# Kernel optimization log

Hardware: AMD Instinct MI355X
Metric: run time of the kernel (lower is better)

Reference implementation:

```python
import math
import jax, jax.numpy as jnp
from jax import lax
import numpy as np

EPS = 1e-07
GAMMA = 2.2
FOV = 10.0
SPEC_ALPHA_MAX = 128.0
SHADOW_CAP = 0.1
SHADOW_SMOOTH = 7


def _grid_sample_border(img, grid):
    # img: [B,1,H,W]; grid: [B,H,W,2], grid[...,0]=x (width), grid[...,1]=y (height),
    # normalized to [-1,1], align_corners=False, padding_mode='border' (torch semantics).
    B, _, H, W = img.shape
    x = (grid[..., 0] + 1.0) * (W / 2.0) - 0.5
    y = (grid[..., 1] + 1.0) * (H / 2.0) - 0.5
    x0 = jnp.floor(x)
    y0 = jnp.floor(y)
    wx = x - x0
    wy = y - y0
    x0i = jnp.clip(x0.astype(jnp.int32), 0, W - 1)
    x1i = jnp.clip(x0.astype(jnp.int32) + 1, 0, W - 1)
    y0i = jnp.clip(y0.astype(jnp.int32), 0, H - 1)
    y1i = jnp.clip(y0.astype(jnp.int32) + 1, 0, H - 1)
    im = img[:, 0]  # [B,H,W]
    bidx = jnp.arange(B)[:, None, None]
    v00 = im[bidx, y0i, x0i]
    v01 = im[bidx, y0i, x1i]
    v10 = im[bidx, y1i, x0i]
    v11 = im[bidx, y1i, x1i]
    out = (v00 * (1 - wx) * (1 - wy) + v01 * wx * (1 - wy)
           + v10 * (1 - wx) * wy + v11 * wx * wy)
    return out[:, None]  # [B,1,H,W]


def compute_shadow(depth, light_dir, fov=FOV):
    # Iterative shadow ray-march: image_size grid_sample steps along -light_dir.
    depth = lax.stop_gradient(depth)          # original detaches
    light_dir = lax.stop_gradient(light_dir)
    B, _, S, _ = depth.shape
    t = math.tan(fov / 360.0 * math.pi)
    c = jnp.linspace(-1.0, 1.0, S, dtype=depth.dtype) * t
    xx, yy = jnp.meshgrid(c, c, indexing='ij')  # torch.meshgrid default ij
    dirs = jnp.stack([yy, xx, jnp.ones_like(xx)], axis=0)[None]  # [1,3,S,S]
    pos0 = dirs * depth                                          # [B,3,S,S]
    step = -light_dir.reshape(B, 3, 1, 1) / S

    def body(i, carry):
        pos, sh = carry
        pos = pos + step
        pix = pos[:, :2] / pos[:, 2:3] / t           # [B,2,S,S]
        grid = jnp.transpose(pix, (0, 2, 3, 1))      # [B,S,S,2]
        sampled = _grid_sample_border(depth, grid)
        sh = sh | (sampled - pos[:, 2:3] < 0)
        return (pos, sh)

    _, sh = lax.fori_loop(0, S, body, (pos0, jnp.zeros(depth.shape, dtype=bool)))
    return sh


def _gaussian_blur(x, ksize=SHADOW_SMOOTH, sigma=2.0):
    r = (ksize - 1) / 2.0
    g = np.exp(-((np.arange(ksize) - r) ** 2) / (2.0 * sigma ** 2))
    k2 = np.outer(g, g)
    k2 = (k2 / k2.sum()).astype(np.float32)
    kern = jnp.asarray(k2)[None, None]  # [1,1,k,k]
    return lax.conv_general_dilated(x, kern, (1, 1), 'SAME',
                                    dimension_numbers=('NCHW', 'OIHW', 'NCHW'))


def _get_view_d(fov, S):
    t = math.tan(fov / 360.0 * math.pi)
    x = jnp.linspace(-1.0, 1.0, S, dtype=jnp.float32) * t
    xx, yy = jnp.meshgrid(x, x, indexing='ij')
    v = jnp.stack([yy, xx, jnp.ones_like(xx)], axis=0)  # [3,S,S]
    v = v / jnp.linalg.norm(v, axis=0, keepdims=True)
    v = v[:, ::-1, ::-1]  # flip([1,2])
    return v[None]  # [1,3,S,S]


def _border_mask(S, margin=5):
    m = jnp.zeros((S, S), dtype=jnp.float32)
    m = m.at[margin:S - margin, margin:S - margin].set(1.0)
    return m[None, None]


def setup_inputs() -> dict:
    key = jax.random.key(0)
    k1, k2, k3, k4, k5 = jax.random.split(key, 5)
    B, S = 32, 256
    netA_out = jax.random.normal(k1, (B, 5, S, S), dtype=jnp.float32)
    netL_out = jax.random.normal(k2, (B, 6), dtype=jnp.float32)
    n = jax.random.normal(k3, (B, 3, S, S), dtype=jnp.float32)
    recon_normal = n / jnp.linalg.norm(n, axis=1, keepdims=True)
    recon_depth = jax.random.uniform(k4, (B, 1, S, S), dtype=jnp.float32) * 0.5 + 0.75
    light = jax.random.normal(k5, (B, 2), dtype=jnp.float32)
    return {"netA_out": netA_out, "netL_out": netL_out,
            "recon_normal": recon_normal, "recon_depth": recon_depth,
            "light": light}


def reference(netA_out, netL_out, recon_normal, recon_depth, light):
    b, _, S, _ = netA_out.shape
    t_alpha = math.sqrt(SPEC_ALPHA_MAX) - 1.0

    recon_albedo_specular = jnp.tanh(netA_out)
    recon_albedo = (recon_albedo_specular[:, :3] / 2 + 0.5) ** GAMMA  # to_gamma_space

    recon_light = jnp.tanh(netL_out)  # [B,6]
    # spec_alpha: tanh of netL_out[:, :1], rescaled to [1, spec_alpha_max]
    sa = jnp.tanh(netL_out[:, :1]).reshape(b, 1, 1, 1)
    spec_alpha = ((sa * 0.5 + 0.5) * t_alpha + 1.0) ** 2
    spec_strength = (recon_light[:, 5:6].reshape(b, 1, 1, 1) * 0.5 + 0.5) * 0.5

    light_a = (recon_light[:, 1:2] / 2 + 0.5).reshape(b, 1, 1, 1)
    light_b = (recon_light[:, 2:3] / 2 + 0.5).reshape(b, 1, 1, 1)
    # light has shape [B,2] -> concat z=1, then normalize
    light_d = jnp.concatenate([light, jnp.ones((b, 1), dtype=light.dtype)], axis=1)
    light_d = light_d / jnp.linalg.norm(light_d, axis=1, keepdims=True)

    view_d = _get_view_d(FOV, S)
    ld = light_d[:, :, None, None]
    cos_theta = jnp.sum(recon_normal * ld, axis=1, keepdims=True)
    diffuse = jnp.clip(cos_theta, 0.0)

    mask = _border_mask(S, 5)
    reflect_d = 2.0 * cos_theta * recon_normal - ld
    specular = (jnp.clip(jnp.sum(view_d * reflect_d, axis=1, keepdims=True), 0.0)
                * (cos_theta > 0).astype(jnp.float32) * mask)
    spec_shading = jnp.clip(specular, EPS, 1.0 - EPS) ** spec_alpha

    is_shadow = compute_shadow(recon_depth, light_d).astype(jnp.float32)
    shadow_s = _gaussian_blur(is_shadow)
    shadow_factor = jnp.clip(1.0 - shadow_s, SHADOW_CAP, 1.0)

    shading = light_a + light_b * diffuse * shadow_factor
    recon_im = recon_albedo * shading + spec_strength * light_b * spec_shading
    recon_im = jnp.clip(recon_im, EPS) ** (1.0 / GAMMA)  # from_gamma_space
    return recon_im
```

## Files before the change

### kernel.cpp

```cpp
#include <hip/hip_runtime.h>


#define SDIM 256
#define SS   (SDIM * SDIM)
#define TAN_T 0.08748866352592401
#define STEPC (2.0f / 255.0f)
#define POOL  1024
#define CPB   64
#define MDV   (0.75f - 1e-6f)

__device__ __forceinline__ bool shadow_test(float px, float py, float pz,
                                            const float* __restrict__ im) {
#pragma clang fp contract(off)
    const float T = (float)TAN_T;
    const float K = (float)(128.0 / TAN_T);
    float inv = __builtin_amdgcn_rcpf(pz);
    inv = fmaf(fmaf(-pz, inv, 1.0f), inv, inv);
    const float xf = fmaf(px * inv, K, 127.5f);
    const float yf = fmaf(py * inv, K, 127.5f);
    const float x0ff = floorf(xf);
    const float y0ff = floorf(yf);
    const float wxf = xf - x0ff;
    const float wyf = yf - y0ff;
    const int x0 = (int)x0ff;
    const int y0 = (int)y0ff;
    const int x0c = min(max(x0, 0), 255), x1c = min(max(x0 + 1, 0), 255);
    const int y0c = min(max(y0, 0), 255), y1c = min(max(y0 + 1, 0), 255);
    const int r0 = y0c << 8, r1 = y1c << 8;
    const float v00 = im[r0 + x0c];
    const float v01 = im[r0 + x1c];
    const float v10 = im[r1 + x0c];
    const float v11 = im[r1 + x1c];
    const float omx = 1.0f - wxf, omy = 1.0f - wyf;
    const float t0 = fmaf(v01, wxf, v00 * omx);
    const float t1 = fmaf(v11, wxf, v10 * omx);
    const float sF = fmaf(t1, wyf, t0 * omy);
    const float diff = sF - pz;
    const float guard = fmaf(fabsf(xf) + fabsf(yf), 6e-7f, 1e-5f);
    bool shf = diff < 0.0f;
    if (__builtin_expect(fabsf(diff) <= guard, 0)) {
        const float gx = (px / pz) / T;
        const float gy = (py / pz) / T;
        const float x = (gx + 1.0f) * 128.0f - 0.5f;
        const float y = (gy + 1.0f) * 128.0f - 0.5f;
        const float xo = floorf(x), yo = floorf(y);
        const float wx = x - xo, wy = y - yo;
        const int ex0 = (int)xo, ey0 = (int)yo;
        const int ex0c = min(max(ex0, 0), 255), ex1c = min(max(ex0 + 1, 0), 255);
        const int ey0c = min(max(ey0, 0), 255), ey1c = min(max(ey0 + 1, 0), 255);
        const float e00 = im[(ey0c << 8) + ex0c];
        const float e01 = im[(ey0c << 8) + ex1c];
        const float e10 = im[(ey1c << 8) + ex0c];
        const float e11 = im[(ey1c << 8) + ex1c];
        float s = e00 * (1.0f - wx) * (1.0f - wy);
        s = s + e01 * wx * (1.0f - wy);
        s = s + e10 * (1.0f - wx) * wy;
        s = s + e11 * wx * wy;
        shf = (s - pz) < 0.0f;
    }
    return shf;
}

__global__ __launch_bounds__(256) void shadow_march(const float* __restrict__ depth,
                                                    const float* __restrict__ light,
                                                    unsigned char* __restrict__ shmap) {
#pragma clang fp contract(off)
    const int blk   = blockIdx.x;
    const int b     = blk >> 6;
    const int chunk = blk & (CPB - 1);
    const int rbase = chunk * POOL;
    const float* im = depth + (size_t)b * SS;
    const int tid = threadIdx.x;
    const int lane = tid & 63;

    const float lx = light[b * 2 + 0];
    const float ly = light[b * 2 + 1];
    float n2 = lx * lx;
    n2 = n2 + ly * ly;
    n2 = n2 + 1.0f;
    const float nr = sqrtf(n2);
    const float sx = (-(lx / nr)) / 256.0f;
    const float sy = (-(ly / nr)) / 256.0f;
    const float sz = (-(1.0f / nr)) / 256.0f;
    const float T = (float)TAN_T;

    __shared__ float         dcache[POOL];
    __shared__ unsigned char res[POOL];
    __shared__ int           popc;
    if (tid == 0) popc = 0;
#pragma unroll
    for (int u = 0; u < POOL / 256; ++u) {
        const int r = tid + u * 256;
        dcache[r] = im[rbase + r];
    }
    __syncthreads();

    bool has = false, done = false, sh = false;
    float px = 0.0f, py = 0.0f, pz = 0.0f;
    int rr = 0, krem = 0;

#pragma unroll 1
    while (true) {
        const bool need = (!has) && (!done);
        const unsigned long long mneed = __ballot(need);
        if (mneed != 0ull) {
            if (need) {
                const int leader = (int)__ffsll(mneed) - 1;
                int base = 0;
                if (lane == leader) base = atomicAdd(&popc, __popcll(mneed));
                base = __shfl(base, leader, 64);
                const int p = base + __popcll(mneed & ((1ull << (unsigned)lane) - 1ull));
                if (p < POOL) {
                    const float d = dcache[p];
                    const int gidx = rbase + p;
                    const int i = gidx >> 8, j = gidx & 255;
                    const float cj = (-1.0f + (float)j * STEPC) * T;
                    const float ci = (-1.0f + (float)i * STEPC) * T;
                    px = cj * d; py = ci * d; pz = d;
                    rr = p; krem = 256; sh = false; has = true;
                } else {
                    done = true;
                }
            }
        }
        if (__ballot(has) == 0ull) break;
        if (has) {
            px += sx; py += sy; pz += sz; --krem;
            bool dead = false;
            if (pz <= MDV) {
                dead = true;
            } else if (shadow_test(px, py, pz, im)) {
                sh = true; dead = true;
            } else if (krem == 0) {
                dead = true;
            }
            if (dead) {
                res[rr] = sh ? (unsigned char)1 : (unsigned char)0;
                has = false;
            }
        }
    }
    __syncthreads();
    ((unsigned int*)(shmap + (size_t)b * SS + rbase))[tid] = ((const unsigned int*)res)[tid];
}

__device__ __constant__ float W1[7] = {
    0.07015933f, 0.13107488f, 0.19071282f, 0.21610594f,
    0.19071282f, 0.13107488f, 0.07015933f
};

__device__ __forceinline__ float fpow(float x, float p) {
    return __builtin_amdgcn_exp2f(p * __builtin_amdgcn_logf(x));
}
__device__ __forceinline__ float ftanh(float x) {
    const float e = __builtin_amdgcn_exp2f(x * 2.8853900817779268f);
    return (e - 1.0f) * __builtin_amdgcn_rcpf(e + 1.0f);
}

__global__ __launch_bounds__(256) void compose_kernel(const float* __restrict__ netA,
                                                      const float* __restrict__ netL,
                                                      const float* __restrict__ nrm,
                                                      const float* __restrict__ light,
                                                      const unsigned char* __restrict__ shmap,
                                                      float* __restrict__ out) {
    __shared__ float tile[22][23];

    const int b  = blockIdx.z;
    const int tx = threadIdx.x & 15;
    const int ty = threadIdx.x >> 4;
    const int j0 = blockIdx.x * 16;
    const int i0 = blockIdx.y * 16;

    const unsigned char* shb = shmap + (size_t)b * SS;
    for (int idx = threadIdx.x; idx < 22 * 22; idx += 256) {
        const int r = idx / 22, c = idx - r * 22;
        const int gi = i0 - 3 + r, gj = j0 - 3 + c;
        float v = 0.0f;
        if (gi >= 0 && gi < SDIM && gj >= 0 && gj < SDIM) v = (float)shb[gi * SDIM + gj];
        tile[r][c] = v;
    }
    __syncthreads();

    const int i = i0 + ty;
    const int j = j0 + tx;

    float shadow_s = 0.0f;
#pragma unroll
    for (int dy = 0; dy < 7; ++dy) {
        float rs = 0.0f;
#pragma unroll
        for (int dx = 0; dx < 7; ++dx) rs += W1[dx] * tile[ty + dy][tx + dx];
        shadow_s += W1[dy] * rs;
    }

    const float l0 = tanhf(netL[b * 6 + 0]);
    const float l1 = tanhf(netL[b * 6 + 1]);
    const float l2 = tanhf(netL[b * 6 + 2]);
    const float l5 = tanhf(netL[b * 6 + 5]);
    const float e  = l0 * 0.5f + 0.5f;
    const float f  = e * (float)10.313708498984761 + 1.0f;
    const float spec_alpha    = f * f;
    const float spec_strength = (l5 * 0.5f + 0.5f) * 0.5f;
    const float light_a = l1 / 2.0f + 0.5f;
    const float light_b = l2 / 2.0f + 0.5f;

    const float lx = light[b * 2 + 0];
    const float ly = light[b * 2 + 1];
    const float ln = sqrtf(lx * lx + ly * ly + 1.0f);
    const float ldx = lx / ln, ldy = ly / ln, ldz = 1.0f / ln;

    const float T = (float)TAN_T;
    const float xsj = (-1.0f + (float)(SDIM - 1 - j) * STEPC) * T;
    const float xsi = (-1.0f + (float)(SDIM - 1 - i) * STEPC) * T;
    const float vn = sqrtf(xsj * xsj + xsi * xsi + 1.0f);
    const float vd0 = xsj / vn, vd1 = xsi / vn, vd2 = 1.0f / vn;

    const size_t pix = (size_t)i * SDIM + j;
    const float n0 = nrm[((size_t)(b * 3 + 0)) * SS + pix];
    const float n1 = nrm[((size_t)(b * 3 + 1)) * SS + pix];
    const float n2 = nrm[((size_t)(b * 3 + 2)) * SS + pix];

    const float cos_t   = n0 * ldx + n1 * ldy + n2 * ldz;
    const float diffuse = fmaxf(cos_t, 0.0f);

    const float r0 = 2.0f * cos_t * n0 - ldx;
    const float r1 = 2.0f * cos_t * n1 - ldy;
    const float r2 = 2.0f * cos_t * n2 - ldz;
    float spec = fmaxf(vd0 * r0 + vd1 * r1 + vd2 * r2, 0.0f);
    const float gate  = (cos_t > 0.0f) ? 1.0f : 0.0f;
    const float maskv = (i >= 5 && i < SDIM - 5 && j >= 5 && j < SDIM - 5) ? 1.0f : 0.0f;
    spec = spec * gate * maskv;
    const float sclip = fminf(fmaxf(spec, 1e-7f), (float)(1.0 - 1e-7));
    const float sshad = fpow(sclip, spec_alpha);

    const float shadow_factor = fminf(fmaxf(1.0f - shadow_s, 0.1f), 1.0f);
    const float shading   = light_a + light_b * diffuse * shadow_factor;
    const float spec_term = spec_strength * light_b * sshad;

    const float inv_g = (float)(1.0 / 2.2);
#pragma unroll
    for (int c = 0; c < 3; ++c) {
        const float a   = netA[((size_t)(b * 5 + c)) * SS + pix];
        const float alb = fpow(ftanh(a) * 0.5f + 0.5f, 2.2f);
        float rim = alb * shading + spec_term;
        rim = fmaxf(rim, 1e-7f);
        out[((size_t)(b * 3 + c)) * SS + pix] = fpow(rim, inv_g);
    }
}

extern "C" void kernel_launch(void* const* d_in, const int* in_sizes, int n_in,
                              void* d_out, int out_size, void* d_ws, size_t ws_size,
                              hipStream_t stream) {
    const float* netA  = (const float*)d_in[0];
    const float* netL  = (const float*)d_in[1];
    const float* nrm   = (const float*)d_in[2];
    const float* depth = (const float*)d_in[3];
    const float* light = (const float*)d_in[4];
    float* out = (float*)d_out;

    unsigned char* shmap = (unsigned char*)d_ws;

    shadow_march<<<32 * CPB, 256, 0, stream>>>(depth, light, shmap);
    compose_kernel<<<dim3(SDIM / 16, SDIM / 16, 32), 256, 0, stream>>>(netA, netL, nrm,
                                                                       light, shmap, out);
}
```

Before: 243.1 us.

## Remap shadow-march blocks to span all batches for one image row segment

Each shadow-march block used to handle 1024 consecutive pixels of a single batch image. Now a block takes a 32-pixel segment of one row across all 32 batches, and loads per-batch light steps and depth image offsets from shared memory. The aim is to even out per-block work, since ray lengths vary with each batch's light direction, so the work-pool and ballot loop face less tail imbalance. In exchange, gathers within a block now touch 32 different depth images, which can hurt cache locality. The output stores also become scattered 4-byte writes.

Result: slower. 260.6 us (+7.2%).

```diff
diff --git a/kernel.cpp b/kernel.cpp
--- a/kernel.cpp
+++ b/kernel.cpp
@@ -6,11 +6,11 @@
 #define TAN_T 0.08748866352592401
 #define STEPC (2.0f / 255.0f)
 #define POOL  1024
-#define CPB   64
 #define MDV   (0.75f - 1e-6f)
 
 __device__ __forceinline__ bool shadow_test(float px, float py, float pz,
-                                            const float* __restrict__ im) {
+                                            const float* __restrict__ depth,
+                                            int ibase) {
 #pragma clang fp contract(off)
     const float T = (float)TAN_T;
     const float K = (float)(128.0 / TAN_T);
@@ -26,11 +26,11 @@
     const int y0 = (int)y0ff;
     const int x0c = min(max(x0, 0), 255), x1c = min(max(x0 + 1, 0), 255);
     const int y0c = min(max(y0, 0), 255), y1c = min(max(y0 + 1, 0), 255);
-    const int r0 = y0c << 8, r1 = y1c << 8;
-    const float v00 = im[r0 + x0c];
-    const float v01 = im[r0 + x1c];
-    const float v10 = im[r1 + x0c];
-    const float v11 = im[r1 + x1c];
+    const int r0 = ibase + (y0c << 8), r1 = ibase + (y1c << 8);
+    const float v00 = depth[r0 + x0c];
+    const float v01 = depth[r0 + x1c];
+    const float v10 = depth[r1 + x0c];
+    const float v11 = depth[r1 + x1c];
     const float omx = 1.0f - wxf, omy = 1.0f - wyf;
     const float t0 = fmaf(v01, wxf, v00 * omx);
     const float t1 = fmaf(v11, wxf, v10 * omx);
@@ -48,10 +48,10 @@
         const int ex0 = (int)xo, ey0 = (int)yo;
         const int ex0c = min(max(ex0, 0), 255), ex1c = min(max(ex0 + 1, 0), 255);
         const int ey0c = min(max(ey0, 0), 255), ey1c = min(max(ey0 + 1, 0), 255);
-        const float e00 = im[(ey0c << 8) + ex0c];
-        const float e01 = im[(ey0c << 8) + ex1c];
-        const float e10 = im[(ey1c << 8) + ex0c];
-        const float e11 = im[(ey1c << 8) + ex1c];
+        const float e00 = depth[ibase + (ey0c << 8) + ex0c];
+        const float e01 = depth[ibase + (ey0c << 8) + ex1c];
+        const float e10 = depth[ibase + (ey1c << 8) + ex0c];
+        const float e11 = depth[ibase + (ey1c << 8) + ex1c];
         float s = e00 * (1.0f - wx) * (1.0f - wy);
         s = s + e01 * wx * (1.0f - wy);
         s = s + e10 * (1.0f - wx) * wy;
@@ -65,39 +65,44 @@
                                                     const float* __restrict__ light,
                                                     unsigned char* __restrict__ shmap) {
 #pragma clang fp contract(off)
-    const int blk   = blockIdx.x;
-    const int b     = blk >> 6;
-    const int chunk = blk & (CPB - 1);
-    const int rbase = chunk * POOL;
-    const float* im = depth + (size_t)b * SS;
-    const int tid = threadIdx.x;
+    const int bk   = blockIdx.x;
+    const int row  = bk >> 3;
+    const int col0 = (bk & 7) << 5;
+    const int tid  = threadIdx.x;
     const int lane = tid & 63;
-
-    const float lx = light[b * 2 + 0];
-    const float ly = light[b * 2 + 1];
-    float n2 = lx * lx;
-    n2 = n2 + ly * ly;
-    n2 = n2 + 1.0f;
-    const float nr = sqrtf(n2);
-    const float sx = (-(lx / nr)) / 256.0f;
-    const float sy = (-(ly / nr)) / 256.0f;
-    const float sz = (-(1.0f / nr)) / 256.0f;
     const float T = (float)TAN_T;
 
     __shared__ float         dcache[POOL];
     __shared__ unsigned char res[POOL];
+    __shared__ float         lsx[32], lsy[32], lsz[32];
     __shared__ int           popc;
     if (tid == 0) popc = 0;
+
+    if (tid < 32) {
+        const float lx = light[tid * 2 + 0];
+        const float ly = light[tid * 2 + 1];
+        float n2 = lx * lx;
+        n2 = n2 + ly * ly;
+        n2 = n2 + 1.0f;
+        const float nr = sqrtf(n2);
+        lsx[tid] = (-(lx / nr)) / 256.0f;
+        lsy[tid] = (-(ly / nr)) / 256.0f;
+        lsz[tid] = (-(1.0f / nr)) / 256.0f;
+    }
 #pragma unroll
     for (int u = 0; u < POOL / 256; ++u) {
-        const int r = tid + u * 256;
-        dcache[r] = im[rbase + r];
+        const int q = tid + (u << 8);
+        const int b = q >> 5;
+        dcache[q] = depth[(size_t)b * SS + (row << 8) + col0 + (q & 31)];
     }
     __syncthreads();
+
+    const float ci = (-1.0f + (float)row * STEPC) * T;
 
     bool has = false, done = false, sh = false;
     float px = 0.0f, py = 0.0f, pz = 0.0f;
-    int rr = 0, krem = 0;
+    float sx = 0.0f, sy = 0.0f, sz = 0.0f;
+    int ibase = 0, rr = 0, krem = 0;
 
 #pragma unroll 1
     while (true) {
@@ -111,11 +116,11 @@
                 base = __shfl(base, leader, 64);
                 const int p = base + __popcll(mneed & ((1ull << (unsigned)lane) - 1ull));
                 if (p < POOL) {
+                    const int b = p >> 5;
                     const float d = dcache[p];
-                    const int gidx = rbase + p;
-                    const int i = gidx >> 8, j = gidx & 255;
-                    const float cj = (-1.0f + (float)j * STEPC) * T;
-                    const float ci = (-1.0f + (float)i * STEPC) * T;
+                    sx = lsx[b]; sy = lsy[b]; sz = lsz[b];
+                    ibase = b << 16;
+                    const float cj = (-1.0f + (float)(col0 + (p & 31)) * STEPC) * T;
                     px = cj * d; py = ci * d; pz = d;
                     rr = p; krem = 256; sh = false; has = true;
                 } else {
@@ -129,7 +134,7 @@
             bool dead = false;
             if (pz <= MDV) {
                 dead = true;
-            } else if (shadow_test(px, py, pz, im)) {
+            } else if (shadow_test(px, py, pz, depth, ibase)) {
                 sh = true; dead = true;
             } else if (krem == 0) {
                 dead = true;
@@ -141,7 +146,12 @@
         }
     }
     __syncthreads();
-    ((unsigned int*)(shmap + (size_t)b * SS + rbase))[tid] = ((const unsigned int*)res)[tid];
+    {
+        const int bb  = tid >> 3;
+        const int off = (tid & 7) << 2;
+        *(unsigned int*)(shmap + (size_t)bb * SS + (row << 8) + col0 + off) =
+            ((const unsigned int*)res)[tid];
+    }
 }
 
 __device__ __constant__ float W1[7] = {
@@ -260,7 +270,7 @@
 
     unsigned char* shmap = (unsigned char*)d_ws;
 
-    shadow_march<<<32 * CPB, 256, 0, stream>>>(depth, light, shmap);
+    shadow_march<<<2048, 256, 0, stream>>>(depth, light, shmap);
     compose_kernel<<<dim3(SDIM / 16, SDIM / 16, 32), 256, 0, stream>>>(netA, netL, nrm,
                                                                        light, shmap, out);
 }
```
